# Kernel optimization log

Measured on AMD Instinct MI355X. Metric: run time of the kernel, lower is better.

Reference implementation:

```python
import jax, jax.numpy as jnp
import numpy as np

F8_MAX = 448.0   # max representable magnitude of float8_e4m3fn
EPS = 1e-12      # amax clamp from the source


def setup_inputs() -> dict:
    key = jax.random.key(0)
    kx, kw, kb = jax.random.split(key, 3)
    B, S, K, N = 8, 8192, 1024, 1024
    x = jax.random.normal(kx, (B, S, K), dtype=jnp.float32)
    weight = jax.random.normal(kw, (N, K), dtype=jnp.float32) * 0.02  # (out, in) like nn.Linear
    bias = jax.random.normal(kb, (N,), dtype=jnp.float32)
    return {"x": x, "weight": weight, "bias": bias}


def _quantize_fp8(t):
    """Per-tensor dynamic fp8-e4m3 quantization: returns (t_fp8, scale)."""
    scale = jnp.maximum(jnp.max(jnp.abs(t)), EPS) / F8_MAX
    t8 = (t / scale).astype(jnp.float8_e4m3fn)
    return t8, scale


def reference(x, weight, bias):
    lead = x.shape[:-1]
    K = x.shape[-1]
    N = weight.shape[0]
    x_flat = x.reshape(-1, K).astype(jnp.float32)

    # dynamic activation quantization (forward-time, per tensor)
    x8, x_scale = _quantize_fp8(x_flat)
    # weight quantization (from_linear, per tensor)
    w8, w_scale = _quantize_fp8(weight.astype(jnp.float32))

    out = jnp.dot(x8.astype(jnp.float32), w8.astype(jnp.float32).T) * (x_scale * w_scale)
    out = out.astype(x.dtype).reshape(*lead, N)
    return out + bias
```

## Files before the change

### kernel.cpp

```cpp
#include <hip/hip_runtime.h>
#include <stdint.h>

#define F8MAX 448.0f
#define QEPS 1e-12f
#define SCL_ONE 0x7F7F7F7F

typedef float floatx16 __attribute__((ext_vector_type(16)));
typedef int   intx4    __attribute__((ext_vector_type(4)));
typedef int   intx8    __attribute__((ext_vector_type(8)));

__global__ void amax_partial(const float* __restrict__ in, int n4, float* __restrict__ partial)
{
    const float4* in4 = (const float4*)in;
    int tid = blockIdx.x * blockDim.x + threadIdx.x;
    int stride = gridDim.x * blockDim.x;
    float m = 0.0f;
    for (int i = tid; i < n4; i += stride) {
        float4 v = in4[i];
        m = fmaxf(m, fmaxf(fmaxf(fabsf(v.x), fabsf(v.y)), fmaxf(fabsf(v.z), fabsf(v.w))));
    }
    #pragma unroll
    for (int off = 32; off > 0; off >>= 1)
        m = fmaxf(m, __shfl_xor(m, off, 64));
    __shared__ float sm[4];
    if ((threadIdx.x & 63) == 0) sm[threadIdx.x >> 6] = m;
    __syncthreads();
    if (threadIdx.x == 0)
        partial[blockIdx.x] = fmaxf(fmaxf(sm[0], sm[1]), fmaxf(sm[2], sm[3]));
}

__global__ void final_reduce(const float* __restrict__ px, int nx,
                             const float* __restrict__ pw, int nw,
                             unsigned* __restrict__ hdr)
{
    float mx = 0.0f, mw = 0.0f;
    for (int i = threadIdx.x; i < nx; i += 256) mx = fmaxf(mx, px[i]);
    for (int i = threadIdx.x; i < nw; i += 256) mw = fmaxf(mw, pw[i]);
    #pragma unroll
    for (int off = 32; off > 0; off >>= 1) {
        mx = fmaxf(mx, __shfl_xor(mx, off, 64));
        mw = fmaxf(mw, __shfl_xor(mw, off, 64));
    }
    __shared__ float sx[4], sw[4];
    if ((threadIdx.x & 63) == 0) { sx[threadIdx.x >> 6] = mx; sw[threadIdx.x >> 6] = mw; }
    __syncthreads();
    if (threadIdx.x == 0) {
        hdr[0] = __float_as_uint(fmaxf(fmaxf(sx[0], sx[1]), fmaxf(sx[2], sx[3])));
        hdr[1] = __float_as_uint(fmaxf(fmaxf(sw[0], sw[1]), fmaxf(sw[2], sw[3])));
    }
}

__global__ void quant_scramble(const float* __restrict__ in, uint8_t* __restrict__ out,
                               const unsigned* __restrict__ hdr, int hidx, int nkt, int K, int rev)
{
    int bid = blockIdx.x;
    if (rev) bid = gridDim.x - 1 - bid;
    int p  = bid / nkt;
    int kt = bid - p * nkt;
    float amax = __uint_as_float(hdr[hidx]);
    float scale = fmaxf(amax, QEPS) / F8MAX;

    uint8_t* dst = out + (size_t)bid * 8192;

    #pragma unroll
    for (int i = 0; i < 2; i++) {
        int idx = threadIdx.x + i * 256;
        int h  = idx >> 8;
        int pc = (idx >> 7) & 1;
        int r  = idx & 127;
        const float* src = in + (size_t)(p * 128 + r) * K + kt * 64 + h * 32 + pc * 16;
        float4 f0 = *(const float4*)(src);
        float4 f1 = *(const float4*)(src + 4);
        float4 f2 = *(const float4*)(src + 8);
        float4 f3 = *(const float4*)(src + 12);
        int w0 = 0, w1 = 0, w2 = 0, w3 = 0;
        w0 = __builtin_amdgcn_cvt_pk_fp8_f32(f0.x / scale, f0.y / scale, w0, false);
        w0 = __builtin_amdgcn_cvt_pk_fp8_f32(f0.z / scale, f0.w / scale, w0, true);
        w1 = __builtin_amdgcn_cvt_pk_fp8_f32(f1.x / scale, f1.y / scale, w1, false);
        w1 = __builtin_amdgcn_cvt_pk_fp8_f32(f1.z / scale, f1.w / scale, w1, true);
        w2 = __builtin_amdgcn_cvt_pk_fp8_f32(f2.x / scale, f2.y / scale, w2, false);
        w2 = __builtin_amdgcn_cvt_pk_fp8_f32(f2.z / scale, f2.w / scale, w2, true);
        w3 = __builtin_amdgcn_cvt_pk_fp8_f32(f3.x / scale, f3.y / scale, w3, false);
        w3 = __builtin_amdgcn_cvt_pk_fp8_f32(f3.z / scale, f3.w / scale, w3, true);
        int4 rv; rv.x = w0; rv.y = w1; rv.z = w2; rv.w = w3;
        *(int4*)(dst + (size_t)idx * 16) = rv;
    }
}

__global__ __launch_bounds__(512, 1) void gemm_fp8_mx(
    const uint8_t* __restrict__ A8, const uint8_t* __restrict__ B8,
    float* __restrict__ C, const float* __restrict__ bias,
    const unsigned* __restrict__ hdr, int N, int nkt, int nbn)
{
    __shared__ uint8_t lsA[3 * 16384];
    __shared__ uint8_t lsB[3 * 16384];

    int nwg = gridDim.x;
    int bid = blockIdx.x;
    if ((nwg & 7) == 0) {
        int chunk = nwg >> 3;
        bid = (blockIdx.x & 7) * chunk + (blockIdx.x >> 3);
    }
    int bm = bid / nbn, bn = bid - bm * nbn;

    int t = threadIdx.x;
    int wave = t >> 6, lane = t & 63;
    int wr = wave >> 2, wc = wave & 3;
    int hl = lane >> 5, l31 = lane & 31;

    const uint8_t* gsrc0; const uint8_t* gsrc1; const uint8_t* gsrc2; const uint8_t* gsrc3;
    uint32_t ld0, ld1, ld2, ld3;
    bool isA = (wave < 4);
    {
        int c0 = wave * 4;
        #pragma unroll
        for (int p = 0; p < 4; p++) {
            int c = c0 + p;
            const uint8_t* g;
            uint32_t l;
            if (c < 16) {
                int h = c >> 3, sub = c & 7;
                g = A8 + (size_t)(bm * 2 + h) * nkt * 8192 + sub * 1024 + lane * 16;
                l = (uint32_t)c * 1024;
            } else {
                int cc = c - 16, h = cc >> 3, sub = cc & 7;
                g = B8 + (size_t)(bn * 2 + h) * nkt * 8192 + sub * 1024 + lane * 16;
                l = (uint32_t)cc * 1024;
            }
            if (p == 0) { gsrc0 = g; ld0 = l; }
            else if (p == 1) { gsrc1 = g; ld1 = l; }
            else if (p == 2) { gsrc2 = g; ld2 = l; }
            else { gsrc3 = g; ld3 = l; }
        }
    }
    uint8_t* lsbase = isA ? lsA : lsB;

#define ISSUE(GP, LO, KT2, B2)                                                   \
    __builtin_amdgcn_global_load_lds(                                            \
        (const __attribute__((address_space(1))) void*)((GP) + (size_t)(KT2) * 8192), \
        (__attribute__((address_space(3))) void*)(lsbase + (B2) * 16384 + (LO)), \
        16, 0, 0)

    const uint8_t* baseA = lsA + wr * 8192 + hl * 4096 + l31 * 16;
    const uint8_t* baseB = lsB + (wc >> 1) * 8192 + hl * 4096 + (wc & 1) * 1024 + l31 * 16;

    floatx16 acc[4][2];
    #pragma unroll
    for (int m = 0; m < 4; m++)
        #pragma unroll
        for (int n = 0; n < 2; n++)
            acc[m][n] = (floatx16)(0.0f);

#define RD8(BASE, OFF) __builtin_shufflevector(                         \
        *(const intx4*)((BASE) + (OFF)),                                \
        *(const intx4*)((BASE) + (OFF) + 2048), 0, 1, 2, 3, 4, 5, 6, 7)

#define MMX(m, n) acc[m][n] = __builtin_amdgcn_mfma_scale_f32_32x32x64_f8f6f4( \
        af[m], bf[n], acc[m][n], 0, 0, 0, SCL_ONE, 0, SCL_ONE)

    ISSUE(gsrc0, ld0, 0, 0); ISSUE(gsrc1, ld1, 0, 0); ISSUE(gsrc2, ld2, 0, 0); ISSUE(gsrc3, ld3, 0, 0);
    ISSUE(gsrc0, ld0, 1, 1); ISSUE(gsrc1, ld1, 1, 1); ISSUE(gsrc2, ld2, 1, 1); ISSUE(gsrc3, ld3, 1, 1);
    asm volatile("s_waitcnt vmcnt(4)" ::: "memory");
    asm volatile("s_barrier" ::: "memory");

    int cur = 0;
    for (int kt = 0; kt < nkt; kt++) {
        bool pf = (kt + 2 < nkt);
        int ib = cur - 1; if (ib < 0) ib += 3;
        const uint8_t* cA = baseA + cur * 16384;
        const uint8_t* cB = baseB + cur * 16384;
        intx8 af[4], bf[2];

        if (pf) { ISSUE(gsrc0, ld0, kt + 2, ib); ISSUE(gsrc1, ld1, kt + 2, ib); }
        af[0] = RD8(cA, 0);
        af[1] = RD8(cA, 512);
        bf[0] = RD8(cB, 0);
        bf[1] = RD8(cB, 512);
        asm volatile("s_barrier" ::: "memory");
        __builtin_amdgcn_s_setprio(1);
        MMX(0, 0); MMX(0, 1); MMX(1, 0); MMX(1, 1);
        __builtin_amdgcn_s_setprio(0);
        asm volatile("s_barrier" ::: "memory");

        if (pf) { ISSUE(gsrc2, ld2, kt + 2, ib); ISSUE(gsrc3, ld3, kt + 2, ib); }
        af[2] = RD8(cA, 1024);
        af[3] = RD8(cA, 1536);
        asm volatile("s_barrier" ::: "memory");
        __builtin_amdgcn_s_setprio(1);
        MMX(2, 0); MMX(2, 1); MMX(3, 0); MMX(3, 1);
        __builtin_amdgcn_s_setprio(0);
        if (pf) asm volatile("s_waitcnt vmcnt(4)" ::: "memory");
        else    asm volatile("s_waitcnt vmcnt(0)" ::: "memory");
        asm volatile("s_barrier" ::: "memory");

        cur++; if (cur == 3) cur = 0;
    }

    float sxv = fmaxf(__uint_as_float(hdr[0]), QEPS) / F8MAX;
    float swv = fmaxf(__uint_as_float(hdr[1]), QEPS) / F8MAX;
    float s = sxv * swv;

    #pragma unroll
    for (int m = 0; m < 4; m++) {
        int row0 = bm * 256 + wr * 128 + m * 32 + 4 * hl;
        #pragma unroll
        for (int n = 0; n < 2; n++) {
            int col = bn * 256 + wc * 64 + n * 32 + l31;
            float bv = bias[col];
            #pragma unroll
            for (int reg = 0; reg < 16; reg++) {
                int row = row0 + (reg & 3) + 8 * (reg >> 2);
                C[(size_t)row * N + col] = acc[m][n][reg] * s + bv;
            }
        }
    }
#undef ISSUE
#undef RD8
#undef MMX
}

extern "C" void kernel_launch(void* const* d_in, const int* in_sizes, int n_in,
                              void* d_out, int out_size, void* d_ws, size_t ws_size,
                              hipStream_t stream)
{
    const float* x    = (const float*)d_in[0];
    const float* w    = (const float*)d_in[1];
    const float* bias = (const float*)d_in[2];
    float* out = (float*)d_out;

    int N = in_sizes[2];
    int K = in_sizes[1] / N;
    int M = in_sizes[0] / K;
    int nx = in_sizes[0];
    int nw = in_sizes[1];
    int nkt = K / 64;

    uint8_t* ws = (uint8_t*)d_ws;
    unsigned* hdr = (unsigned*)ws;
    float* px = (float*)(ws + 64);
    float* pw = (float*)(ws + 64 + 4096);
    uint8_t* w8 = ws + 16384;
    uint8_t* x8 = ws + 16384 + (size_t)N * K;

    const int AX_BLOCKS = 1024;
    const int AW_BLOCKS = 256;

    amax_partial<<<AX_BLOCKS, 256, 0, stream>>>(x, nx / 4, px);
    amax_partial<<<AW_BLOCKS, 256, 0, stream>>>(w, nw / 4, pw);
    final_reduce<<<1, 256, 0, stream>>>(px, AX_BLOCKS, pw, AW_BLOCKS, hdr);

    quant_scramble<<<(M / 128) * nkt, 256, 0, stream>>>(x, x8, hdr, 0, nkt, K, 1);
    quant_scramble<<<(N / 128) * nkt, 256, 0, stream>>>(w, w8, hdr, 1, nkt, K, 0);

    int nbm = M / 256, nbn = N / 256;
    gemm_fp8_mx<<<nbm * nbn, 512, 0, stream>>>(x8, w8, out, bias, hdr, N, nkt, nbn);
}
```

Measured before the change: 245.3 us.

## Fuse amax and fp8 quantization into one cooperative kernel; simplify GEMM loop barriers

Replaces the five pre-GEMM launches (two amax partials, final reduce, two quantize passes) with one cooperative kernel that reduces amax, synchronizes the grid, and then quantizes x and w in the same launch. The reverse tile order for x is kept so recently read tiles may still be in cache. The GEMM main loop issues all prefetches up front and drops the intermediate barriers between the two MFMA halves, keeping one barrier per k-step. Output stores become nontemporal. The grid-wide sync relies on all 1024 blocks being co-resident, and the fewer barriers change how waves interleave in the GEMM.

```diff
diff --git a/kernel.cpp b/kernel.cpp
--- a/kernel.cpp
+++ b/kernel.cpp
@@ -1,5 +1,8 @@
 #include <hip/hip_runtime.h>
+#include <hip/hip_cooperative_groups.h>
 #include <stdint.h>
+
+namespace cg = cooperative_groups;
 
 #define F8MAX 448.0f
 #define QEPS 1e-12f
@@ -9,59 +12,12 @@
 typedef int   intx4    __attribute__((ext_vector_type(4)));
 typedef int   intx8    __attribute__((ext_vector_type(8)));
 
-__global__ void amax_partial(const float* __restrict__ in, int n4, float* __restrict__ partial)
-{
-    const float4* in4 = (const float4*)in;
-    int tid = blockIdx.x * blockDim.x + threadIdx.x;
-    int stride = gridDim.x * blockDim.x;
-    float m = 0.0f;
-    for (int i = tid; i < n4; i += stride) {
-        float4 v = in4[i];
-        m = fmaxf(m, fmaxf(fmaxf(fabsf(v.x), fabsf(v.y)), fmaxf(fabsf(v.z), fabsf(v.w))));
-    }
-    #pragma unroll
-    for (int off = 32; off > 0; off >>= 1)
-        m = fmaxf(m, __shfl_xor(m, off, 64));
-    __shared__ float sm[4];
-    if ((threadIdx.x & 63) == 0) sm[threadIdx.x >> 6] = m;
-    __syncthreads();
-    if (threadIdx.x == 0)
-        partial[blockIdx.x] = fmaxf(fmaxf(sm[0], sm[1]), fmaxf(sm[2], sm[3]));
-}
-
-__global__ void final_reduce(const float* __restrict__ px, int nx,
-                             const float* __restrict__ pw, int nw,
-                             unsigned* __restrict__ hdr)
-{
-    float mx = 0.0f, mw = 0.0f;
-    for (int i = threadIdx.x; i < nx; i += 256) mx = fmaxf(mx, px[i]);
-    for (int i = threadIdx.x; i < nw; i += 256) mw = fmaxf(mw, pw[i]);
-    #pragma unroll
-    for (int off = 32; off > 0; off >>= 1) {
-        mx = fmaxf(mx, __shfl_xor(mx, off, 64));
-        mw = fmaxf(mw, __shfl_xor(mw, off, 64));
-    }
-    __shared__ float sx[4], sw[4];
-    if ((threadIdx.x & 63) == 0) { sx[threadIdx.x >> 6] = mx; sw[threadIdx.x >> 6] = mw; }
-    __syncthreads();
-    if (threadIdx.x == 0) {
-        hdr[0] = __float_as_uint(fmaxf(fmaxf(sx[0], sx[1]), fmaxf(sx[2], sx[3])));
-        hdr[1] = __float_as_uint(fmaxf(fmaxf(sw[0], sw[1]), fmaxf(sw[2], sw[3])));
-    }
-}
-
-__global__ void quant_scramble(const float* __restrict__ in, uint8_t* __restrict__ out,
-                               const unsigned* __restrict__ hdr, int hidx, int nkt, int K, int rev)
-{
-    int bid = blockIdx.x;
-    if (rev) bid = gridDim.x - 1 - bid;
-    int p  = bid / nkt;
-    int kt = bid - p * nkt;
-    float amax = __uint_as_float(hdr[hidx]);
-    float scale = fmaxf(amax, QEPS) / F8MAX;
-
-    uint8_t* dst = out + (size_t)bid * 8192;
-
+__device__ __forceinline__ void quant_tile(const float* __restrict__ in, uint8_t* __restrict__ out,
+                                           int tile, float scale, int nkt, int K)
+{
+    int p  = tile / nkt;
+    int kt = tile - p * nkt;
+    uint8_t* dst = out + (size_t)tile * 8192;
     #pragma unroll
     for (int i = 0; i < 2; i++) {
         int idx = threadIdx.x + i * 256;
@@ -85,6 +41,70 @@
         int4 rv; rv.x = w0; rv.y = w1; rv.z = w2; rv.w = w3;
         *(int4*)(dst + (size_t)idx * 16) = rv;
     }
+}
+
+__global__ __launch_bounds__(256) void fused_amax_quant(
+    const float* __restrict__ x, const float* __restrict__ w,
+    uint8_t* __restrict__ x8, uint8_t* __restrict__ w8,
+    float* __restrict__ px, float* __restrict__ pw, unsigned* __restrict__ hdr,
+    int nx4, int nw4, int ntx, int ntw, int nkt, int K)
+{
+    cg::grid_group grid = cg::this_grid();
+
+    int tid = blockIdx.x * 256 + threadIdx.x;
+    int stride = gridDim.x * 256;
+    const float4* x4 = (const float4*)x;
+    const float4* w4 = (const float4*)w;
+    float mx = 0.f, mw = 0.f;
+    for (int i = tid; i < nx4; i += stride) {
+        float4 v = x4[i];
+        mx = fmaxf(mx, fmaxf(fmaxf(fabsf(v.x), fabsf(v.y)), fmaxf(fabsf(v.z), fabsf(v.w))));
+    }
+    for (int i = tid; i < nw4; i += stride) {
+        float4 v = w4[i];
+        mw = fmaxf(mw, fmaxf(fmaxf(fabsf(v.x), fabsf(v.y)), fmaxf(fabsf(v.z), fabsf(v.w))));
+    }
+    #pragma unroll
+    for (int off = 32; off; off >>= 1) {
+        mx = fmaxf(mx, __shfl_xor(mx, off, 64));
+        mw = fmaxf(mw, __shfl_xor(mw, off, 64));
+    }
+    __shared__ float smx[4], smw[4];
+    if ((threadIdx.x & 63) == 0) { smx[threadIdx.x >> 6] = mx; smw[threadIdx.x >> 6] = mw; }
+    __syncthreads();
+    if (threadIdx.x == 0) {
+        px[blockIdx.x] = fmaxf(fmaxf(smx[0], smx[1]), fmaxf(smx[2], smx[3]));
+        pw[blockIdx.x] = fmaxf(fmaxf(smw[0], smw[1]), fmaxf(smw[2], smw[3]));
+    }
+
+    grid.sync();
+
+    float gx = 0.f, gw = 0.f;
+    for (int i = threadIdx.x; i < (int)gridDim.x; i += 256) {
+        gx = fmaxf(gx, px[i]);
+        gw = fmaxf(gw, pw[i]);
+    }
+    #pragma unroll
+    for (int off = 32; off; off >>= 1) {
+        gx = fmaxf(gx, __shfl_xor(gx, off, 64));
+        gw = fmaxf(gw, __shfl_xor(gw, off, 64));
+    }
+    __syncthreads();
+    if ((threadIdx.x & 63) == 0) { smx[threadIdx.x >> 6] = gx; smw[threadIdx.x >> 6] = gw; }
+    __syncthreads();
+    float ax = fmaxf(fmaxf(smx[0], smx[1]), fmaxf(smx[2], smx[3]));
+    float aw = fmaxf(fmaxf(smw[0], smw[1]), fmaxf(smw[2], smw[3]));
+    if (blockIdx.x == 0 && threadIdx.x == 0) {
+        hdr[0] = __float_as_uint(ax);
+        hdr[1] = __float_as_uint(aw);
+    }
+    float sclx = fmaxf(ax, QEPS) / F8MAX;
+    float sclw = fmaxf(aw, QEPS) / F8MAX;
+
+    for (int t = blockIdx.x; t < ntx; t += gridDim.x)
+        quant_tile(x, x8, ntx - 1 - t, sclx, nkt, K);
+    for (int t = blockIdx.x; t < ntw; t += gridDim.x)
+        quant_tile(w, w8, t, sclw, nkt, K);
 }
 
 __global__ __launch_bounds__(512, 1) void gemm_fp8_mx(
@@ -171,28 +191,23 @@
         const uint8_t* cB = baseB + cur * 16384;
         intx8 af[4], bf[2];
 
-        if (pf) { ISSUE(gsrc0, ld0, kt + 2, ib); ISSUE(gsrc1, ld1, kt + 2, ib); }
-        af[0] = RD8(cA, 0);
-        af[1] = RD8(cA, 512);
-        bf[0] = RD8(cB, 0);
-        bf[1] = RD8(cB, 512);
-        asm volatile("s_barrier" ::: "memory");
+        if (pf) { ISSUE(gsrc0, ld0, kt + 2, ib); ISSUE(gsrc1, ld1, kt + 2, ib);
+                  ISSUE(gsrc2, ld2, kt + 2, ib); ISSUE(gsrc3, ld3, kt + 2, ib); }
+
+        af[0] = RD8(cA, 0);    af[1] = RD8(cA, 512);
+        bf[0] = RD8(cB, 0);    bf[1] = RD8(cB, 512);
+        af[2] = RD8(cA, 1024); af[3] = RD8(cA, 1536);
+
         __builtin_amdgcn_s_setprio(1);
         MMX(0, 0); MMX(0, 1); MMX(1, 0); MMX(1, 1);
-        __builtin_amdgcn_s_setprio(0);
-        asm volatile("s_barrier" ::: "memory");
-
-        if (pf) { ISSUE(gsrc2, ld2, kt + 2, ib); ISSUE(gsrc3, ld3, kt + 2, ib); }
-        af[2] = RD8(cA, 1024);
-        af[3] = RD8(cA, 1536);
-        asm volatile("s_barrier" ::: "memory");
-        __builtin_amdgcn_s_setprio(1);
         MMX(2, 0); MMX(2, 1); MMX(3, 0); MMX(3, 1);
         __builtin_amdgcn_s_setprio(0);
-        if (pf) asm volatile("s_waitcnt vmcnt(4)" ::: "memory");
-        else    asm volatile("s_waitcnt vmcnt(0)" ::: "memory");
-        asm volatile("s_barrier" ::: "memory");
-
+
+        if (kt + 1 < nkt) {
+            if (pf) asm volatile("s_waitcnt vmcnt(4)" ::: "memory");
+            else    asm volatile("s_waitcnt vmcnt(0)" ::: "memory");
+            asm volatile("s_barrier" ::: "memory");
+        }
         cur++; if (cur == 3) cur = 0;
     }
 
@@ -210,7 +225,7 @@
             #pragma unroll
             for (int reg = 0; reg < 16; reg++) {
                 int row = row0 + (reg & 3) + 8 * (reg >> 2);
-                C[(size_t)row * N + col] = acc[m][n][reg] * s + bv;
+                __builtin_nontemporal_store(acc[m][n][reg] * s + bv, &C[(size_t)row * N + col]);
             }
         }
     }
@@ -242,15 +257,18 @@
     uint8_t* w8 = ws + 16384;
     uint8_t* x8 = ws + 16384 + (size_t)N * K;
 
-    const int AX_BLOCKS = 1024;
-    const int AW_BLOCKS = 256;
-
-    amax_partial<<<AX_BLOCKS, 256, 0, stream>>>(x, nx / 4, px);
-    amax_partial<<<AW_BLOCKS, 256, 0, stream>>>(w, nw / 4, pw);
-    final_reduce<<<1, 256, 0, stream>>>(px, AX_BLOCKS, pw, AW_BLOCKS, hdr);
-
-    quant_scramble<<<(M / 128) * nkt, 256, 0, stream>>>(x, x8, hdr, 0, nkt, K, 1);
-    quant_scramble<<<(N / 128) * nkt, 256, 0, stream>>>(w, w8, hdr, 1, nkt, K, 0);
+    int nx4 = nx / 4, nw4 = nw / 4;
+    int ntx = (M / 128) * nkt;
+    int ntw = (N / 128) * nkt;
+    int Kv = K;
+
+    const float* xa = x; const float* wa = w;
+    uint8_t* x8a = x8; uint8_t* w8a = w8;
+    float* pxa = px; float* pwa = pw; unsigned* hdra = hdr;
+    void* args[] = { &xa, &wa, &x8a, &w8a, &pxa, &pwa, &hdra,
+                     &nx4, &nw4, &ntx, &ntw, &nkt, &Kv };
+    hipLaunchCooperativeKernel((void*)fused_amax_quant, dim3(1024), dim3(256),
+                               args, 0, stream);
 
     int nbm = M / 256, nbn = N / 256;
     gemm_fp8_mx<<<nbm * nbn, 512, 0, stream>>>(x8, w8, out, bias, hdr, N, nkt, nbn);
```

Result: slower. 322.8 us (+31.6%).
